# Kernel tuning notes

Measured on AMD Instinct MI355X. Metric: run time of the kernel, lower is better.

Reference implementation:

```python
import jax, jax.numpy as jnp
import numpy as np

WS = 7        # window size (cubic)
SHIFT = 3     # shift size (cubic)
NH = 6        # num heads
EPS = 1e-5


def _layernorm(x, g, b):
    m = x.mean(-1, keepdims=True)
    v = ((x - m) ** 2).mean(-1, keepdims=True)
    return (x - m) / jnp.sqrt(v + EPS) * g + b


def _win_partition(x, ws):
    # (B,H,W,T,C) -> (B*nW, ws^3, C)
    B, H, W, T, C = x.shape
    x = x.reshape(B, H // ws, ws, W // ws, ws, T // ws, ws, C)
    return x.transpose(0, 1, 3, 5, 2, 4, 6, 7).reshape(-1, ws * ws * ws, C)


def _win_reverse(w, ws, B, H, W, T):
    # (B*nW, ws^3, C) -> (B,H,W,T,C)
    C = w.shape[-1]
    x = w.reshape(B, H // ws, W // ws, T // ws, ws, ws, ws, C)
    return x.transpose(0, 1, 4, 2, 5, 3, 6, 7).reshape(B, H, W, T, C)


def _rel_index(ws):
    # 3D relative position index, (N, N) int, N = ws^3 (torch.meshgrid default 'ij')
    coords = np.stack(np.meshgrid(np.arange(ws), np.arange(ws), np.arange(ws), indexing='ij'))
    cf = coords.reshape(3, -1)
    rel = (cf[:, :, None] - cf[:, None, :]).transpose(1, 2, 0)
    rel[:, :, 0] += ws - 1
    rel[:, :, 1] += ws - 1
    rel[:, :, 2] += ws - 1
    rel[:, :, 0] *= (2 * ws - 1) ** 2
    rel[:, :, 1] *= (2 * ws - 1)
    return rel.sum(-1)


def _compute_mask(Hp, Wp, Tp, ws, shift):
    img = np.zeros((1, Hp, Wp, Tp, 1), np.float32)
    cnt = 0
    sl = (slice(0, -ws), slice(-ws, -shift), slice(-shift, None))
    for h in sl:
        for w in sl:
            for t in sl:
                img[:, h, w, t, :] = cnt
                cnt += 1
    mw = np.asarray(_win_partition(jnp.asarray(img), ws)).reshape(-1, ws ** 3)  # (nW, N)
    am = mw[:, None, :] - mw[:, :, None]
    return jnp.asarray(np.where(am != 0, -100.0, 0.0).astype(np.float32))


def setup_inputs() -> dict:
    key = jax.random.key(0)
    ks = jax.random.split(key, 10)
    B, Hd, Wd, Td, C = 2, 28, 28, 28, 192
    L = Hd * Wd * Td
    Ch = int(C * 4.0)
    s = 0.02
    inp = {
        'x': jax.random.normal(ks[0], (B, L, C), jnp.float32),
        'mask': _compute_mask(Hd, Wd, Td, WS, SHIFT),
        'gamma1': jnp.ones((C,), jnp.float32),
        'beta1': jnp.zeros((C,), jnp.float32),
        'qkv_w': jax.random.normal(ks[1], (3 * C, C), jnp.float32) * s,
        'qkv_b': jnp.zeros((3 * C,), jnp.float32),
        'rpb_table': jax.random.normal(ks[2], ((2 * WS - 1) ** 3, NH), jnp.float32) * s,
        'proj_w': jax.random.normal(ks[3], (C, C), jnp.float32) * s,
        'proj_b': jnp.zeros((C,), jnp.float32),
        'gamma2': jnp.ones((C,), jnp.float32),
        'beta2': jnp.zeros((C,), jnp.float32),
        'fc1_w': jax.random.normal(ks[4], (Ch, C), jnp.float32) * s,
        'fc1_b': jnp.zeros((Ch,), jnp.float32),
        'fc2_w': jax.random.normal(ks[5], (C, Ch), jnp.float32) * s,
        'fc2_b': jnp.zeros((C,), jnp.float32),
        'H': Hd, 'W': Wd, 'T': Td,
    }
    return inp


def reference(x, mask, gamma1, beta1, qkv_w, qkv_b, rpb_table, proj_w, proj_b,
              gamma2, beta2, fc1_w, fc1_b, fc2_w, fc2_b, H, W, T):
    B, L, C = x.shape
    hd = C // NH
    scale = hd ** -0.5
    shortcut = x

    h1 = _layernorm(x, gamma1, beta1).reshape(B, H, W, T, C)
    # H,W,T are multiples of WS -> no padding; cyclic shift for SW-MSA
    shifted = jnp.roll(h1, (-SHIFT, -SHIFT, -SHIFT), axis=(1, 2, 3))
    xw = _win_partition(shifted, WS)            # (B*nW, N, C)
    Bn, N, _ = xw.shape

    qkv = (xw @ qkv_w.T + qkv_b).reshape(Bn, N, 3, NH, hd).transpose(2, 0, 3, 1, 4)
    q, k, v = qkv[0] * scale, qkv[1], qkv[2]     # (Bn, NH, N, hd)
    attn = jnp.einsum('bhnd,bhmd->bhnm', q, k)   # (Bn, NH, N, N)

    idx = _rel_index(WS)
    bias = rpb_table[idx.reshape(-1)].reshape(N, N, NH).transpose(2, 0, 1)
    attn = attn + bias[None]

    nW = mask.shape[0]
    attn = attn.reshape(Bn // nW, nW, NH, N, N) + mask[None, :, None]
    attn = jax.nn.softmax(attn.reshape(Bn, NH, N, N), axis=-1)

    out = jnp.einsum('bhnm,bhmd->bhnd', attn, v).transpose(0, 2, 1, 3).reshape(Bn, N, C)
    out = out @ proj_w.T + proj_b

    shifted = _win_reverse(out, WS, B, H, W, T)
    xr = jnp.roll(shifted, (SHIFT, SHIFT, SHIFT), axis=(1, 2, 3)).reshape(B, L, C)

    x = shortcut + xr
    h2 = _layernorm(x, gamma2, beta2)
    m = jax.nn.gelu(h2 @ fc1_w.T + fc1_b, approximate=False)
    return x + (m @ fc2_w.T + fc2_b)
```

## Files before the change

### kernel.cpp

```cpp
#include <hip/hip_runtime.h>
#include <hip/hip_bf16.h>

typedef unsigned short u16;
typedef unsigned int u32;
typedef __attribute__((ext_vector_type(8))) short s16x8;
typedef __attribute__((ext_vector_type(4))) float f32x4;

__device__ __forceinline__ u16 f2bf(float f) {
    union { float f; u32 u; } x; x.f = f;
    u32 r = x.u + 0x7fffu + ((x.u >> 16) & 1u);
    return (u16)(r >> 16);
}
__device__ __forceinline__ float bflo(u32 v) {
    union { u32 u; float f; } x; x.u = v << 16; return x.f;
}
__device__ __forceinline__ float bfhi(u32 v) {
    union { u32 u; float f; } x; x.u = v & 0xffff0000u; return x.f;
}
__device__ __forceinline__ u32 cvt_pk_bf16(float a, float b) {
    u32 r;
    asm("v_cvt_pk_bf16_f32 %0, %1, %2" : "=v"(r) : "v"(a), "v"(b));
    return r;
}
__device__ __forceinline__ void gl2lds(const u16* g, u16* l) {
    __builtin_amdgcn_global_load_lds(
        (const __attribute__((address_space(1))) unsigned int*)g,
        (__attribute__((address_space(3))) unsigned int*)l, 16, 0, 0);
}

#define L_TOK 21952
#define C_DIM 192
#define LOG2E 1.4426950408889634f
#define Q2SCALE 0.2550565444463649f
#define BT_STR 352

__global__ __launch_bounds__(256) void cvt_k(const float* __restrict__ s0,
                                             const float* __restrict__ s1,
                                             const float* __restrict__ s2,
                                             const float* __restrict__ s3,
                                             u16* __restrict__ dst)
{
    int i = blockIdx.x * 256 + threadIdx.x;
    float v;
    if (i < 110592) v = s0[i];
    else if (i < 147456) v = s1[i - 110592];
    else if (i < 294912) v = s2[i - 147456];
    else v = s3[i - 294912];
    dst[i] = f2bf(v);
}

__global__ __launch_bounds__(256) void bias48_k(const float* __restrict__ rpb,
                                                u16* __restrict__ biasT)
{
    const int gid = blockIdx.x * 256 + threadIdx.x;
    const int z = gid / 30976;
    const int rem = gid - z * 30976;
    const int m = rem / 88;
    const int n0 = (rem - m * 88) * 4;
    const int hh = z >> 3, wt = z & 7;

    u16 v[4];
    if (m <= 342) {
        const int hm = m / 49, r2 = m - hm * 49, wm = r2 / 7, tm = r2 - wm * 7;
        const int rm = ((wt & 4) ? (hm < 4 ? 1 : 2) : 0) * 9
                     + ((wt & 2) ? (wm < 4 ? 1 : 2) : 0) * 3
                     + ((wt & 1) ? (tm < 4 ? 1 : 2) : 0);
        #pragma unroll
        for (int j = 0; j < 4; j++) {
            const int n = n0 + j;
            float b = -100000.0f;
            if (n <= 342) {
                int hq = n / 49, r1 = n - hq * 49, wq = r1 / 7, tq = r1 - wq * 7;
                int idx = ((hq - hm + 6) * 13 + (wq - wm + 6)) * 13 + (tq - tm + 6);
                b = rpb[idx * 6 + hh];
                int rq = ((wt & 4) ? (hq < 4 ? 1 : 2) : 0) * 9
                       + ((wt & 2) ? (wq < 4 ? 1 : 2) : 0) * 3
                       + ((wt & 1) ? (tq < 4 ? 1 : 2) : 0);
                if (rq != rm) b -= 100.0f;
                b *= LOG2E;
            }
            v[j] = f2bf(b);
        }
    } else {
        const u16 neg = f2bf(-100000.0f);
        v[0] = neg; v[1] = neg; v[2] = neg; v[3] = neg;
    }
    u32 lo = (u32)v[0] | ((u32)v[1] << 16);
    u32 hi = (u32)v[2] | ((u32)v[3] << 16);
    *(uint2*)&biasT[((size_t)z * 352 + m) * BT_STR + n0] = (uint2){lo, hi};
}

template<int MODE>
__global__ __launch_bounds__(256) void ln_k(const float* __restrict__ in,
                                            const float* __restrict__ g,
                                            const float* __restrict__ b,
                                            u16* __restrict__ out)
{
    const int lane = threadIdx.x & 63, wv = threadIdx.x >> 6;
    const int tok = blockIdx.x * 4 + wv;
    size_t base = (size_t)tok * C_DIM;
    float x0 = in[base + lane];
    float x1 = in[base + 64 + lane];
    float x2 = in[base + 128 + lane];
    float s = x0 + x1 + x2;
    float sq = x0 * x0 + x1 * x1 + x2 * x2;
    #pragma unroll
    for (int off = 32; off > 0; off >>= 1) {
        s += __shfl_xor(s, off, 64);
        sq += __shfl_xor(sq, off, 64);
    }
    const float mean = s * (1.0f / 192.0f);
    float var = sq * (1.0f / 192.0f) - mean * mean;
    var = fmaxf(var, 0.0f);
    const float rstd = rsqrtf(var + 1e-5f);

    size_t obase;
    if (MODE == 0) {
        int bi = tok / L_TOK;
        int l = tok - bi * L_TOK;
        int h = l / 784;
        int rm = l - h * 784;
        int w = rm / 28;
        int t = rm - w * 28;
        int hs = h + 25; if (hs >= 28) hs -= 28;
        int ws = w + 25; if (ws >= 28) ws -= 28;
        int ts = t + 25; if (ts >= 28) ts -= 28;
        int win = ((bi * 4 + hs / 7) * 4 + ws / 7) * 4 + ts / 7;
        int n = (hs % 7) * 49 + (ws % 7) * 7 + (ts % 7);
        obase = ((size_t)win * 343 + n) * C_DIM;
    } else {
        obase = base;
    }
    #pragma unroll
    for (int i = 0; i < 3; i++) {
        int c = lane + i * 64;
        float xv = (i == 0) ? x0 : (i == 1) ? x1 : x2;
        float y = (xv - mean) * rstd * g[c] + b[c];
        out[obase + c] = f2bf(y);
    }
}

template<int K, int EPI, int NX>
__global__ __launch_bounds__(256, 8) void gemm64_k(const u16* __restrict__ A,
                                                   const u16* __restrict__ W,
                                                   const float* __restrict__ bias,
                                                   void* __restrict__ outp,
                                                   const void* __restrict__ resp,
                                                   int Ncols)
{
    constexpr int NC = K / 64;
    __shared__ __align__(16) u16 As[2][4096];
    __shared__ __align__(16) u16 Bs[2][4096];
    const int t = threadIdx.x;
    constexpr int NWG = NX * 686;
    constexpr int QQ = NWG >> 3, RR = NWG & 7;
    const int orig = blockIdx.x;
    const int xcd = orig & 7, rnk = orig >> 3;
    const int wgid = (xcd < RR ? xcd * (QQ + 1) : RR * (QQ + 1) + (xcd - RR) * QQ) + rnk;
    const int bm = wgid / NX;
    const int n0 = (wgid - bm * NX) * 64;

    const int lane = t & 63, wv = t >> 6;
    const int r16 = lane & 15, quad = lane >> 4;
    const int ar = t >> 2, ac = (t & 3) * 8;
    const size_t abase = (size_t)bm * 64 * K;

    f32x4 acc[4];
    #pragma unroll
    for (int fn = 0; fn < 4; fn++) acc[fn] = (f32x4){0.f, 0.f, 0.f, 0.f};

    auto STAGE = [&](int c, int b) {
        #pragma unroll
        for (int kt = 0; kt < 2; kt++) {
            gl2lds(&A[abase + (size_t)ar * K + c * 64 + kt * 32 + ac], &As[b][kt * 2048 + 8 * t]);
            gl2lds(&W[(size_t)(n0 + ar) * K + c * 64 + kt * 32 + ac], &Bs[b][kt * 2048 + 8 * t]);
        }
    };

    STAGE(0, 0);
    for (int c = 0; c < NC; ++c) {
        const int cur = c & 1;
        if (c + 1 < NC) {
            STAGE(c + 1, cur ^ 1);
            asm volatile("s_waitcnt vmcnt(4)" ::: "memory");
        } else {
            asm volatile("s_waitcnt vmcnt(0)" ::: "memory");
        }
        __builtin_amdgcn_s_barrier();
        __builtin_amdgcn_sched_barrier(0);
        #pragma unroll
        for (int kt = 0; kt < 2; kt++) {
            s16x8 af = *(const s16x8*)&As[cur][kt * 2048 + (wv * 16 + r16) * 32 + quad * 8];
            #pragma unroll
            for (int fn = 0; fn < 4; fn++) {
                s16x8 bf = *(const s16x8*)&Bs[cur][kt * 2048 + (fn * 16 + r16) * 32 + quad * 8];
                acc[fn] = __builtin_amdgcn_mfma_f32_16x16x32_bf16(af, bf, acc[fn], 0, 0, 0);
            }
        }
        __builtin_amdgcn_s_barrier();
    }

    #pragma unroll
    for (int r = 0; r < 4; r++) {
        const int grow = bm * 64 + wv * 16 + quad * 4 + r;
        size_t rowbase = (size_t)grow * ((EPI == 2) ? C_DIM : Ncols);
        #pragma unroll
        for (int fn = 0; fn < 4; fn++) {
            const int gcol = n0 + fn * 16 + r16;
            float v = acc[fn][r] + bias[gcol];
            if (EPI == 0) {
                if (gcol < 192) v *= Q2SCALE;
                ((u16*)outp)[rowbase + gcol] = f2bf(v);
            } else if (EPI == 1) {
                v = 0.5f * v * (1.0f + erff(v * 0.70710678118654752f));
                ((u16*)outp)[rowbase + gcol] = f2bf(v);
            } else {
                size_t o = rowbase + gcol;
                ((float*)outp)[o] = v + ((const float*)resp)[o];
            }
        }
    }
}

__global__ __launch_bounds__(256) void projln_k(const u16* __restrict__ A,
                                                const u16* __restrict__ W,
                                                const float* __restrict__ bias,
                                                const float* __restrict__ res,
                                                const float* __restrict__ g2,
                                                const float* __restrict__ b2,
                                                float* __restrict__ x2,
                                                u16* __restrict__ h2)
{
    constexpr int K = 192, NC = 3;
    __shared__ __align__(16) u16 As[2][4096];
    __shared__ __align__(16) u16 Bs[2][12288];
    const int t = threadIdx.x, bm = blockIdx.x;
    const int lane = t & 63, wv = t >> 6;
    const int r16 = lane & 15, quad = lane >> 4;
    const int ar = t >> 2, ac = (t & 3) * 8;
    const size_t abase = (size_t)bm * 64 * K;

    f32x4 acc[12];
    #pragma unroll
    for (int fn = 0; fn < 12; fn++) acc[fn] = (f32x4){0.f, 0.f, 0.f, 0.f};

    auto STAGE = [&](int c, int b) {
        #pragma unroll
        for (int kt = 0; kt < 2; kt++) {
            gl2lds(&A[abase + (size_t)ar * K + c * 64 + kt * 32 + ac], &As[b][kt * 2048 + 8 * t]);
            #pragma unroll
            for (int bb = 0; bb < 3; bb++)
                gl2lds(&W[(size_t)(bb * 64 + ar) * K + c * 64 + kt * 32 + ac],
                       &Bs[b][kt * 6144 + bb * 2048 + 8 * t]);
        }
    };

    STAGE(0, 0);
    for (int c = 0; c < NC; ++c) {
        const int cur = c & 1;
        if (c + 1 < NC) {
            STAGE(c + 1, cur ^ 1);
            asm volatile("s_waitcnt vmcnt(8)" ::: "memory");
        } else {
            asm volatile("s_waitcnt vmcnt(0)" ::: "memory");
        }
        __builtin_amdgcn_s_barrier();
        __builtin_amdgcn_sched_barrier(0);
        #pragma unroll
        for (int kt = 0; kt < 2; kt++) {
            s16x8 af = *(const s16x8*)&As[cur][kt * 2048 + (wv * 16 + r16) * 32 + quad * 8];
            #pragma unroll
            for (int fn = 0; fn < 12; fn++) {
                s16x8 bf = *(const s16x8*)&Bs[cur][kt * 6144 + (fn * 16 + r16) * 32 + quad * 8];
                acc[fn] = __builtin_amdgcn_mfma_f32_16x16x32_bf16(af, bf, acc[fn], 0, 0, 0);
            }
        }
        __builtin_amdgcn_s_barrier();
    }

    #pragma unroll
    for (int r = 0; r < 4; r++) {
        const int grow = bm * 64 + wv * 16 + quad * 4 + r;
        int win = grow / 343, n = grow - win * 343;
        int bi = win >> 6, wi = win & 63;
        int hw = wi >> 4, ww = (wi >> 2) & 3, tw = wi & 3;
        int ph = n / 49, rem = n - ph * 49;
        int pw = rem / 7, pt = rem - pw * 7;
        int h = hw * 7 + ph + 3; if (h >= 28) h -= 28;
        int w = ww * 7 + pw + 3; if (w >= 28) w -= 28;
        int tt = tw * 7 + pt + 3; if (tt >= 28) tt -= 28;
        int l = (h * 28 + w) * 28 + tt;
        size_t rowbase = ((size_t)bi * L_TOK + l) * C_DIM;

        float y[12];
        float s = 0.f, sq = 0.f;
        #pragma unroll
        for (int fn = 0; fn < 12; fn++) {
            const int gcol = fn * 16 + r16;
            float v = acc[fn][r] + bias[gcol] + res[rowbase + gcol];
            y[fn] = v; s += v; sq += v * v;
        }
        #pragma unroll
        for (int off = 1; off < 16; off <<= 1) {
            s += __shfl_xor(s, off, 64);
            sq += __shfl_xor(sq, off, 64);
        }
        const float mean = s * (1.0f / 192.0f);
        float var = sq * (1.0f / 192.0f) - mean * mean;
        var = fmaxf(var, 0.0f);
        const float rstd = rsqrtf(var + 1e-5f);
        #pragma unroll
        for (int fn = 0; fn < 12; fn++) {
            const int gcol = fn * 16 + r16;
            x2[rowbase + gcol] = y[fn];
            h2[rowbase + gcol] = f2bf((y[fn] - mean) * rstd * g2[gcol] + b2[gcol]);
        }
    }
}

__global__ __launch_bounds__(256, 3) void attn_k(const u16* __restrict__ qkv,
                                                 const u16* __restrict__ biasAll,
                                                 u16* __restrict__ out)
{
    __shared__ __align__(16) u16 Ks[352 * 32];
    __shared__ __align__(16) u16 Vt[32 * 360];
    __shared__ __align__(16) u16 Pb[4][16 * 40];

    const int hh = blockIdx.x;
    const int win = blockIdx.y;
    const int wi = win & 63;
    const int t = threadIdx.x, lane = t & 63, wv = t >> 6;
    const int r16 = lane & 15, quad = lane >> 4;
    const size_t qbase = (size_t)win * 343 * 576 + hh * 32;

    for (int j = t; j < 343 * 4; j += 256) {
        int m = j >> 2, ch = j & 3;
        *(uint4*)&Ks[m * 32 + ch * 8] = *(const uint4*)&qkv[qbase + (size_t)m * 576 + 192 + ch * 8];
    }
    if (t < 36) {
        int m = 343 + (t >> 2), ch = t & 3;
        *(uint4*)&Ks[m * 32 + ch * 8] = (uint4){0u, 0u, 0u, 0u};
    }
    for (int i = t; i < 343 * 16; i += 256) {
        int m = i >> 4, d2 = (i & 15) * 2;
        int pm = (m & ~31) + 2 * (m & 15) + ((m >> 4) & 1);
        u32 w2 = *(const u32*)&qkv[qbase + (size_t)m * 576 + 384 + d2];
        Vt[d2 * 360 + pm] = (u16)(w2 & 0xffffu);
        Vt[(d2 + 1) * 360 + pm] = (u16)(w2 >> 16);
    }
    for (int i = t; i < 32 * 9; i += 256) {
        int d = i / 9, m = 343 + i % 9;
        int pm = (m & ~31) + 2 * (m & 15) + ((m >> 4) & 1);
        Vt[d * 360 + pm] = 0;
    }
    __syncthreads();

    const int wt = (((wi >> 4) == 3) ? 4 : 0) | ((((wi >> 2) & 3) == 3) ? 2 : 0)
                 | (((wi & 3) == 3) ? 1 : 0);
    const u16* biashT = biasAll + (size_t)(hh * 8 + wt) * 352 * BT_STR;

    s16x8 onesb;
    #pragma unroll
    for (int j = 0; j < 8; j++) onesb[j] = (short)0x3f80;

    for (int qt = 0; qt < 6; qt++) {
        const int row0 = qt * 64 + wv * 16;
        if (row0 > 342) continue;
        int qrow = row0 + r16; if (qrow > 342) qrow = 342;
        s16x8 qa = *(const s16x8*)&qkv[qbase + (size_t)qrow * 576 + quad * 8];

        const int n0 = row0 + quad * 4;

        f32x4 sacc[22];
        #pragma unroll
        for (int fn = 0; fn < 22; fn++) {
            const int col = fn * 16 + r16;
            uint2 bv = *(const uint2*)&biashT[(size_t)col * BT_STR + n0];
            sacc[fn][0] = bflo(bv.x);
            sacc[fn][1] = bfhi(bv.x);
            sacc[fn][2] = bflo(bv.y);
            sacc[fn][3] = bfhi(bv.y);
        }
        #pragma unroll
        for (int fn = 0; fn < 22; fn++) {
            s16x8 kb = *(const s16x8*)&Ks[(fn * 16 + r16) * 32 + quad * 8];
            sacc[fn] = __builtin_amdgcn_mfma_f32_16x16x32_bf16(qa, kb, sacc[fn], 0, 0, 0);
        }

        #pragma unroll
        for (int fn = 0; fn < 22; fn++) {
            #pragma unroll
            for (int r = 0; r < 4; r++)
                sacc[fn][r] = exp2f(fminf(sacc[fn][r], 42.0f));
        }

        u16* pw = &Pb[wv][0];
        u32* pw32 = (u32*)pw;
        f32x4 oacc0 = (f32x4){0.f, 0.f, 0.f, 0.f};
        f32x4 oacc1 = (f32x4){0.f, 0.f, 0.f, 0.f};
        f32x4 osum  = (f32x4){0.f, 0.f, 0.f, 0.f};
        #pragma unroll
        for (int c = 0; c < 11; c++) {
            asm volatile("s_waitcnt lgkmcnt(0)" ::: "memory");
            #pragma unroll
            for (int r = 0; r < 4; r++)
                pw32[(quad * 4 + r) * 20 + r16] = cvt_pk_bf16(sacc[2 * c][r], sacc[2 * c + 1][r]);
            asm volatile("s_waitcnt lgkmcnt(0)" ::: "memory");
            s16x8 pa = *(const s16x8*)&pw[r16 * 40 + quad * 8];
            s16x8 vb0 = *(const s16x8*)&Vt[r16 * 360 + c * 32 + quad * 8];
            s16x8 vb1 = *(const s16x8*)&Vt[(16 + r16) * 360 + c * 32 + quad * 8];
            oacc0 = __builtin_amdgcn_mfma_f32_16x16x32_bf16(pa, vb0, oacc0, 0, 0, 0);
            oacc1 = __builtin_amdgcn_mfma_f32_16x16x32_bf16(pa, vb1, oacc1, 0, 0, 0);
            osum  = __builtin_amdgcn_mfma_f32_16x16x32_bf16(pa, onesb, osum, 0, 0, 0);
        }

        #pragma unroll
        for (int r = 0; r < 4; r++) {
            const int n = n0 + r;
            if (n < 343) {
                const float rs = osum[r];
                const float inv = rs > 0.0f ? 1.0f / rs : 0.0f;
                size_t o = ((size_t)win * 343 + n) * C_DIM + hh * 32;
                out[o + r16] = f2bf(oacc0[r] * inv);
                out[o + 16 + r16] = f2bf(oacc1[r] * inv);
            }
        }
    }
}

extern "C" void kernel_launch(void* const* d_in, const int* in_sizes, int n_in,
                              void* d_out, int out_size, void* d_ws, size_t ws_size,
                              hipStream_t stream)
{
    const float* x      = (const float*)d_in[0];
    const float* g1     = (const float*)d_in[2];
    const float* b1     = (const float*)d_in[3];
    const float* qkv_w  = (const float*)d_in[4];
    const float* qkv_b  = (const float*)d_in[5];
    const float* rpb    = (const float*)d_in[6];
    const float* proj_w = (const float*)d_in[7];
    const float* proj_b = (const float*)d_in[8];
    const float* g2     = (const float*)d_in[9];
    const float* b2     = (const float*)d_in[10];
    const float* fc1_w  = (const float*)d_in[11];
    const float* fc1_b  = (const float*)d_in[12];
    const float* fc2_w  = (const float*)d_in[13];
    const float* fc2_b  = (const float*)d_in[14];

    char* ws = (char*)d_ws;
    u16* xw        = (u16*)(ws + 0);
    u16* biasT     = (u16*)(ws + 0);
    u16* h2        = (u16*)(ws + 0);
    u16* qkv       = (u16*)(ws + 16861184);
    u16* a1        = (u16*)(ws + 16861184);
    u16* attn_out  = (u16*)(ws + 67444736);
    float* x2      = (float*)(ws + 84305920);
    u16* wbf       = (u16*)(ws + 118028288);
    u16* qkv_wb = wbf;
    u16* proj_wb = wbf + 110592;
    u16* fc1_wb = wbf + 147456;
    u16* fc2_wb = wbf + 294912;

    cvt_k<<<dim3(1728), 256, 0, stream>>>(qkv_w, proj_w, fc1_w, fc2_w, wbf);
    ln_k<0><<<dim3(10976), 256, 0, stream>>>(x, g1, b1, xw);
    gemm64_k<192, 0, 9><<<dim3(9 * 686), 256, 0, stream>>>(xw, qkv_wb, qkv_b, qkv, nullptr, 576);
    bias48_k<<<dim3(5808), 256, 0, stream>>>(rpb, biasT);
    attn_k<<<dim3(6, 128), 256, 0, stream>>>(qkv, biasT, attn_out);
    projln_k<<<dim3(686), 256, 0, stream>>>(attn_out, proj_wb, proj_b, x, g2, b2, x2, h2);
    gemm64_k<192, 1, 12><<<dim3(12 * 686), 256, 0, stream>>>(h2, fc1_wb, fc1_b, a1, nullptr, 768);
    gemm64_k<768, 2, 3><<<dim3(3 * 686), 256, 0, stream>>>(a1, fc2_wb, fc2_b, d_out, x2, 192);
}
```

Before: 320.1 us.

## Fuse MLP fc1+GELU+fc2 into one kernel keeping hidden activations in LDS

Replaces the separate fc1 (GELU) and fc2 (residual) GEMM launches with a single mlp_k kernel. Each block computes a 64-row tile of the 768-wide hidden activation into shared memory and then runs fc2 on it directly, so the bf16 hidden tensor never round-trips through global memory. The fc2 weights are stored in a permuted K order to match the packed layout of the hidden tile in LDS. In exchange, each block uses about 144KB of LDS, which allows only one block per CU, and the weight loads are serialized with barriers and no double buffering, so latency hiding drops.

```diff
diff --git a/kernel.cpp b/kernel.cpp
--- a/kernel.cpp
+++ b/kernel.cpp
@@ -42,11 +42,18 @@
 {
     int i = blockIdx.x * 256 + threadIdx.x;
     float v;
+    int o = i;
     if (i < 110592) v = s0[i];
     else if (i < 147456) v = s1[i - 110592];
     else if (i < 294912) v = s2[i - 147456];
-    else v = s3[i - 294912];
-    dst[i] = f2bf(v);
+    else {
+        int j = i - 294912;
+        v = s3[j];
+        int n = j / 768, k = j - n * 768;
+        int kp = (k & ~31) + 2 * (k & 15) + ((k >> 4) & 1);
+        o = 294912 + n * 768 + kp;
+    }
+    dst[o] = f2bf(v);
 }
 
 __global__ __launch_bounds__(256) void bias48_k(const float* __restrict__ rpb,
@@ -90,7 +97,6 @@
     *(uint2*)&biasT[((size_t)z * 352 + m) * BT_STR + n0] = (uint2){lo, hi};
 }
 
-template<int MODE>
 __global__ __launch_bounds__(256) void ln_k(const float* __restrict__ in,
                                             const float* __restrict__ g,
                                             const float* __restrict__ b,
@@ -114,23 +120,19 @@
     var = fmaxf(var, 0.0f);
     const float rstd = rsqrtf(var + 1e-5f);
 
-    size_t obase;
-    if (MODE == 0) {
-        int bi = tok / L_TOK;
-        int l = tok - bi * L_TOK;
-        int h = l / 784;
-        int rm = l - h * 784;
-        int w = rm / 28;
-        int t = rm - w * 28;
-        int hs = h + 25; if (hs >= 28) hs -= 28;
-        int ws = w + 25; if (ws >= 28) ws -= 28;
-        int ts = t + 25; if (ts >= 28) ts -= 28;
-        int win = ((bi * 4 + hs / 7) * 4 + ws / 7) * 4 + ts / 7;
-        int n = (hs % 7) * 49 + (ws % 7) * 7 + (ts % 7);
-        obase = ((size_t)win * 343 + n) * C_DIM;
-    } else {
-        obase = base;
-    }
+    int bi = tok / L_TOK;
+    int l = tok - bi * L_TOK;
+    int h = l / 784;
+    int rm = l - h * 784;
+    int w = rm / 28;
+    int t = rm - w * 28;
+    int hs = h + 25; if (hs >= 28) hs -= 28;
+    int ws = w + 25; if (ws >= 28) ws -= 28;
+    int ts = t + 25; if (ts >= 28) ts -= 28;
+    int win = ((bi * 4 + hs / 7) * 4 + ws / 7) * 4 + ts / 7;
+    int n = (hs % 7) * 49 + (ws % 7) * 7 + (ts % 7);
+    size_t obase = ((size_t)win * 343 + n) * C_DIM;
+
     #pragma unroll
     for (int i = 0; i < 3; i++) {
         int c = lane + i * 64;
@@ -140,12 +142,11 @@
     }
 }
 
-template<int K, int EPI, int NX>
+template<int K, int NX>
 __global__ __launch_bounds__(256, 8) void gemm64_k(const u16* __restrict__ A,
                                                    const u16* __restrict__ W,
                                                    const float* __restrict__ bias,
-                                                   void* __restrict__ outp,
-                                                   const void* __restrict__ resp,
+                                                   u16* __restrict__ outp,
                                                    int Ncols)
 {
     constexpr int NC = K / 64;
@@ -203,21 +204,13 @@
     #pragma unroll
     for (int r = 0; r < 4; r++) {
         const int grow = bm * 64 + wv * 16 + quad * 4 + r;
-        size_t rowbase = (size_t)grow * ((EPI == 2) ? C_DIM : Ncols);
+        size_t rowbase = (size_t)grow * Ncols;
         #pragma unroll
         for (int fn = 0; fn < 4; fn++) {
             const int gcol = n0 + fn * 16 + r16;
             float v = acc[fn][r] + bias[gcol];
-            if (EPI == 0) {
-                if (gcol < 192) v *= Q2SCALE;
-                ((u16*)outp)[rowbase + gcol] = f2bf(v);
-            } else if (EPI == 1) {
-                v = 0.5f * v * (1.0f + erff(v * 0.70710678118654752f));
-                ((u16*)outp)[rowbase + gcol] = f2bf(v);
-            } else {
-                size_t o = rowbase + gcol;
-                ((float*)outp)[o] = v + ((const float*)resp)[o];
-            }
+            if (gcol < 192) v *= Q2SCALE;
+            outp[rowbase + gcol] = f2bf(v);
         }
     }
 }
@@ -314,6 +307,111 @@
             const int gcol = fn * 16 + r16;
             x2[rowbase + gcol] = y[fn];
             h2[rowbase + gcol] = f2bf((y[fn] - mean) * rstd * g2[gcol] + b2[gcol]);
+        }
+    }
+}
+
+__global__ __launch_bounds__(256) void mlp_k(const u16* __restrict__ A,
+                                             const u16* __restrict__ W1,
+                                             const float* __restrict__ bias1,
+                                             const u16* __restrict__ W2p,
+                                             const float* __restrict__ bias2,
+                                             const float* __restrict__ res,
+                                             float* __restrict__ out)
+{
+    __shared__ __align__(16) u16 As[12288];
+    __shared__ __align__(16) u16 Ws[12288];
+    __shared__ __align__(16) u16 Hs[49152];
+    const int t = threadIdx.x, bm = blockIdx.x;
+    const int lane = t & 63, wv = t >> 6;
+    const int r16 = lane & 15, quad = lane >> 4;
+    const int tr = t >> 2, tc = (t & 3) * 8;
+
+    #pragma unroll
+    for (int j = 0; j < 6; j++)
+        gl2lds(&A[((size_t)bm * 64 + tr) * 192 + j * 32 + tc], &As[j * 2048 + 8 * t]);
+    #pragma unroll
+    for (int j = 0; j < 6; j++)
+        gl2lds(&W1[(size_t)tr * 192 + j * 32 + tc], &Ws[j * 2048 + 8 * t]);
+    __syncthreads();
+
+    u32* hs32 = (u32*)Hs;
+    const int hrow = wv * 16 + quad * 4;
+    for (int hc = 0; hc < 12; hc++) {
+        f32x4 acc[4];
+        #pragma unroll
+        for (int fn = 0; fn < 4; fn++) acc[fn] = (f32x4){0.f, 0.f, 0.f, 0.f};
+        #pragma unroll
+        for (int kt = 0; kt < 6; kt++) {
+            s16x8 af = *(const s16x8*)&As[kt * 2048 + (wv * 16 + r16) * 32 + quad * 8];
+            #pragma unroll
+            for (int fn = 0; fn < 4; fn++) {
+                s16x8 bf = *(const s16x8*)&Ws[kt * 2048 + (fn * 16 + r16) * 32 + quad * 8];
+                acc[fn] = __builtin_amdgcn_mfma_f32_16x16x32_bf16(af, bf, acc[fn], 0, 0, 0);
+            }
+        }
+        #pragma unroll
+        for (int g = 0; g < 2; g++) {
+            const float b0 = bias1[hc * 64 + g * 32 + r16];
+            const float b1v = bias1[hc * 64 + g * 32 + 16 + r16];
+            #pragma unroll
+            for (int r = 0; r < 4; r++) {
+                float v0 = acc[2 * g][r] + b0;
+                float v1 = acc[2 * g + 1][r] + b1v;
+                v0 = 0.5f * v0 * (1.0f + erff(v0 * 0.70710678118654752f));
+                v1 = 0.5f * v1 * (1.0f + erff(v1 * 0.70710678118654752f));
+                hs32[(2 * hc + g) * 1024 + (hrow + r) * 16 + r16] = cvt_pk_bf16(v0, v1);
+            }
+        }
+        if (hc < 11) {
+            __syncthreads();
+            #pragma unroll
+            for (int j = 0; j < 6; j++)
+                gl2lds(&W1[(size_t)((hc + 1) * 64 + tr) * 192 + j * 32 + tc], &Ws[j * 2048 + 8 * t]);
+            __syncthreads();
+        }
+    }
+    __syncthreads();
+
+    #pragma unroll
+    for (int j = 0; j < 6; j++) {
+        int kt = j / 3, rr = (j % 3) * 64 + tr;
+        gl2lds(&W2p[(size_t)rr * 768 + kt * 32 + tc], &Ws[j * 2048 + 8 * t]);
+    }
+    __syncthreads();
+
+    f32x4 acc2[12];
+    #pragma unroll
+    for (int fn = 0; fn < 12; fn++) acc2[fn] = (f32x4){0.f, 0.f, 0.f, 0.f};
+    for (int kc = 0; kc < 12; kc++) {
+        #pragma unroll
+        for (int kt = 0; kt < 2; kt++) {
+            s16x8 af = *(const s16x8*)&Hs[(kc * 2 + kt) * 2048 + (wv * 16 + r16) * 32 + quad * 8];
+            #pragma unroll
+            for (int fn = 0; fn < 12; fn++) {
+                s16x8 bf = *(const s16x8*)&Ws[kt * 6144 + (fn * 16 + r16) * 32 + quad * 8];
+                acc2[fn] = __builtin_amdgcn_mfma_f32_16x16x32_bf16(af, bf, acc2[fn], 0, 0, 0);
+            }
+        }
+        if (kc < 11) {
+            __syncthreads();
+            #pragma unroll
+            for (int j = 0; j < 6; j++) {
+                int kt = j / 3, rr = (j % 3) * 64 + tr;
+                gl2lds(&W2p[(size_t)rr * 768 + (kc + 1) * 64 + kt * 32 + tc], &Ws[j * 2048 + 8 * t]);
+            }
+            __syncthreads();
+        }
+    }
+
+    #pragma unroll
+    for (int r = 0; r < 4; r++) {
+        size_t rowbase = ((size_t)bm * 64 + wv * 16 + quad * 4 + r) * C_DIM;
+        #pragma unroll
+        for (int fn = 0; fn < 12; fn++) {
+            const int gcol = fn * 16 + r16;
+            size_t o = rowbase + gcol;
+            out[o] = acc2[fn][r] + bias2[gcol] + res[o];
         }
     }
 }
@@ -452,7 +550,6 @@
     u16* biasT     = (u16*)(ws + 0);
     u16* h2        = (u16*)(ws + 0);
     u16* qkv       = (u16*)(ws + 16861184);
-    u16* a1        = (u16*)(ws + 16861184);
     u16* attn_out  = (u16*)(ws + 67444736);
     float* x2      = (float*)(ws + 84305920);
     u16* wbf       = (u16*)(ws + 118028288);
@@ -462,11 +559,10 @@
     u16* fc2_wb = wbf + 294912;
 
     cvt_k<<<dim3(1728), 256, 0, stream>>>(qkv_w, proj_w, fc1_w, fc2_w, wbf);
-    ln_k<0><<<dim3(10976), 256, 0, stream>>>(x, g1, b1, xw);
-    gemm64_k<192, 0, 9><<<dim3(9 * 686), 256, 0, stream>>>(xw, qkv_wb, qkv_b, qkv, nullptr, 576);
+    ln_k<<<dim3(10976), 256, 0, stream>>>(x, g1, b1, xw);
+    gemm64_k<192, 9><<<dim3(9 * 686), 256, 0, stream>>>(xw, qkv_wb, qkv_b, qkv, 576);
     bias48_k<<<dim3(5808), 256, 0, stream>>>(rpb, biasT);
     attn_k<<<dim3(6, 128), 256, 0, stream>>>(qkv, biasT, attn_out);
     projln_k<<<dim3(686), 256, 0, stream>>>(attn_out, proj_wb, proj_b, x, g2, b2, x2, h2);
-    gemm64_k<192, 1, 12><<<dim3(12 * 686), 256, 0, stream>>>(h2, fc1_wb, fc1_b, a1, nullptr, 768);
-    gemm64_k<768, 2, 3><<<dim3(3 * 686), 256, 0, stream>>>(a1, fc2_wb, fc2_b, d_out, x2, 192);
-}
+    mlp_k<<<dim3(686), 256, 0, stream>>>(h2, fc1_wb, fc1_b, fc2_wb, fc2_b, x2, (float*)d_out);
+}
```

Result: slower. 378.6 us (+18.3%).
